# Performance work log

Measured on AMD Instinct MI355X. Metric: run time of the kernel, lower is better.

The kernel has to match this reference:

```python
import jax, jax.numpy as jnp
import numpy as np

N = 100000   # nodes
E = 3200000  # edges (avg degree 32)
D0, D1, D2, OUT = 128, 64, 64, 10


def setup_inputs() -> dict:
    key = jax.random.key(0)
    ks = jax.random.split(key, 6)
    x = jax.random.normal(ks[0], (N, D0), jnp.float32)
    edge_index = jax.random.randint(ks[1], (2, E), 0, N, jnp.int32)
    Wa1 = jax.random.normal(ks[2], (D0, D1), jnp.float32) / np.sqrt(D0).astype(np.float32)
    ba1 = jnp.zeros((D1,), jnp.float32)
    Wa2 = jax.random.normal(ks[3], (D1, D2), jnp.float32) / np.sqrt(D1).astype(np.float32)
    ba2 = jnp.zeros((D2,), jnp.float32)
    Wl = jax.random.normal(ks[4], (D2 * D2, OUT), jnp.float32) / np.sqrt(D2 * D2).astype(np.float32)
    bl = jnp.zeros((OUT,), jnp.float32)
    return {"x": x, "edge_index": edge_index, "Wa1": Wa1, "ba1": ba1,
            "Wa2": Wa2, "ba2": ba2, "Wl": Wl, "bl": bl}


def _gcn(x, W, b, src, dst, norm):
    # GCNConv: D^{-1/2} (A+I) D^{-1/2} X W + b  (self-loops already in src/dst)
    h = x @ W                                  # [N, Dout]
    m = h[src] * norm[:, None]                 # gather + scale  [E+N, Dout]
    return jax.ops.segment_sum(m, dst, num_segments=N) + b


def reference(x, edge_index, Wa1, ba1, Wa2, ba2, Wl, bl):
    loops = jnp.arange(N, dtype=edge_index.dtype)
    src = jnp.concatenate([edge_index[0], loops])
    dst = jnp.concatenate([edge_index[1], loops])
    deg = jax.ops.segment_sum(jnp.ones_like(src, jnp.float32), dst, num_segments=N)
    dinv = jax.lax.rsqrt(deg)                  # deg >= 1 thanks to self-loops
    norm = dinv[src] * dinv[dst]

    a1 = _gcn(x, Wa1, ba1, src, dst, norm)
    a2 = _gcn(a1, Wa2, ba2, src, dst, norm)
    # Original reuses gcn_a1/gcn_a2 for the x-path, so x_2 == a_2 exactly.
    x2 = a2
    h = a2.T @ x2                              # [D2, D2] attention-style readout
    o = h.reshape(1, -1) @ Wl + bl             # [1, OUT]
    return jax.nn.softmax(o, axis=-1)
```

## Files before the change

### kernel.cpp

```cpp
#include <hip/hip_runtime.h>


#define CHUNK 4096
#define BSH   8

__global__ __launch_bounds__(256) void hist_pass(const int* __restrict__ dst,
                                                 int* __restrict__ ghist,
                                                 int E, int nblk, int nbuck) {
    __shared__ int lcnt[512];
    const int blk = blockIdx.x;
    for (int i = threadIdx.x; i < nbuck; i += 256) lcnt[i] = 0;
    __syncthreads();
    const int base = blk * CHUNK;
    const int end  = min(base + CHUNK, E);
    for (int e = base + threadIdx.x; e < end; e += 256) {
        int d = __builtin_nontemporal_load(&dst[e]);
        atomicAdd(&lcnt[d >> BSH], 1);
    }
    __syncthreads();
    for (int b = threadIdx.x; b < nbuck; b += 256)
        ghist[(size_t)b * nblk + blk] = lcnt[b];
}

__global__ __launch_bounds__(256) void scan_blocks(int* __restrict__ ghist,
                                                   int* __restrict__ btot, int nblk) {
    __shared__ int sh[256];
    int* g = ghist + (size_t)blockIdx.x * nblk;
    const int tid = threadIdx.x;
    int carry = 0;
    for (int base = 0; base < nblk; base += 256) {
        int i = base + tid;
        int v = (i < nblk) ? g[i] : 0;
        sh[tid] = v;
        __syncthreads();
        for (int off = 1; off < 256; off <<= 1) {
            int t = (tid >= off) ? sh[tid - off] : 0;
            __syncthreads();
            sh[tid] += t;
            __syncthreads();
        }
        if (i < nblk) g[i] = carry + sh[tid] - v;
        int tot = sh[255];
        __syncthreads();
        carry += tot;
    }
    if (tid == 0) btot[blockIdx.x] = carry;
}

__global__ void scan_bstart(const int* __restrict__ btot, int* __restrict__ bstart, int nb) {
    __shared__ int sh[512];
    const int tid = threadIdx.x;
    int v = (tid < nb) ? btot[tid] : 0;
    sh[tid] = v;
    __syncthreads();
    for (int off = 1; off < 512; off <<= 1) {
        int t = (tid >= off) ? sh[tid - off] : 0;
        __syncthreads();
        sh[tid] += t;
        __syncthreads();
    }
    if (tid < nb) bstart[tid] = sh[tid] - v;
}

__global__ __launch_bounds__(256) void place_pass(const int* __restrict__ src,
                                                  const int* __restrict__ dst,
                                                  const int* __restrict__ ghist,
                                                  const int* __restrict__ bstart,
                                                  uint2* __restrict__ bedges,
                                                  int E, int nblk, int nbuck) {
    __shared__ int off[512];
    const int blk = blockIdx.x;
    for (int b = threadIdx.x; b < nbuck; b += 256)
        off[b] = bstart[b] + ghist[(size_t)b * nblk + blk];
    __syncthreads();
    const int base = blk * CHUNK;
    const int end  = min(base + CHUNK, E);
    for (int e = base + threadIdx.x; e < end; e += 256) {
        int d = __builtin_nontemporal_load(&dst[e]);
        int s = __builtin_nontemporal_load(&src[e]);
        int pos = atomicAdd(&off[d >> BSH], 1);
        bedges[pos] = make_uint2((unsigned)s, (unsigned)(d & 255));
    }
}

__global__ __launch_bounds__(256) void bucket_csr(const uint2* __restrict__ bedges,
                                                  const int* __restrict__ btot,
                                                  const int* __restrict__ bstart,
                                                  float* __restrict__ dinv,
                                                  int* __restrict__ rowptr,
                                                  int* __restrict__ rowend,
                                                  int* __restrict__ ssorted, int N) {
    __shared__ int lcnt[256];
    __shared__ int sc[256];
    __shared__ int lcur[256];
    const int b   = blockIdx.x;
    const int tid = threadIdx.x;
    const int cnt  = btot[b];
    const int base = bstart[b];
    lcnt[tid] = 0;
    __syncthreads();
    for (int i = tid; i < cnt; i += 256)
        atomicAdd(&lcnt[(int)bedges[base + i].y], 1);
    __syncthreads();
    int c = lcnt[tid];
    sc[tid] = c;
    __syncthreads();
    for (int off = 1; off < 256; off <<= 1) {
        int t = (tid >= off) ? sc[tid - off] : 0;
        __syncthreads();
        sc[tid] += t;
        __syncthreads();
    }
    const int excl = sc[tid] - c;
    const int n = (b << BSH) + tid;
    if (n < N) {
        dinv[n]   = rsqrtf((float)c + 1.0f);
        rowptr[n] = base + excl;
        rowend[n] = base + excl + c;
    }
    lcur[tid] = excl;
    __syncthreads();
    for (int i = tid; i < cnt; i += 256) {
        uint2 e = bedges[base + i];
        int pos = atomicAdd(&lcur[(int)e.y], 1);
        ssorted[base + pos] = (int)e.x;
    }
}

template <int K>
__global__ __launch_bounds__(256) void gemm_tiled(const float* __restrict__ A,
                                                  const float* __restrict__ W,
                                                  const float* __restrict__ dinv,
                                                  float* __restrict__ H, int N) {
    constexpr int KC = 32;
    __shared__ float xs[64][KC + 4];
    __shared__ float ws[KC][64];
    const int tid  = threadIdx.x;
    const int tx   = tid & 15;
    const int ty   = tid >> 4;
    const int base = blockIdx.x * 64;

    float acc[4][4] = {{0.f}};

    for (int kc = 0; kc < K; kc += KC) {
        for (int idx = tid; idx < 512; idx += 256) {
            int node = idx >> 3, k4 = idx & 7;
            int n = base + node;
            float4 v = make_float4(0.f, 0.f, 0.f, 0.f);
            if (n < N) v = *(const float4*)&A[(long long)n * K + kc + k4 * 4];
            *(float4*)&xs[node][k4 * 4] = v;
        }
        for (int idx = tid; idx < 512; idx += 256) {
            int k = idx >> 4, c4 = idx & 15;
            *(float4*)&ws[k][c4 * 4] = *(const float4*)&W[(long long)(kc + k) * 64 + c4 * 4];
        }
        __syncthreads();

#pragma unroll
        for (int k = 0; k < KC; k += 4) {
            float4 xv[4], wv[4];
#pragma unroll
            for (int i = 0; i < 4; ++i) xv[i] = *(const float4*)&xs[ty * 4 + i][k];
#pragma unroll
            for (int j = 0; j < 4; ++j) wv[j] = *(const float4*)&ws[k + j][tx * 4];
#pragma unroll
            for (int i = 0; i < 4; ++i) {
                float xi[4] = {xv[i].x, xv[i].y, xv[i].z, xv[i].w};
#pragma unroll
                for (int j = 0; j < 4; ++j) {
                    acc[i][0] += xi[j] * wv[j].x;
                    acc[i][1] += xi[j] * wv[j].y;
                    acc[i][2] += xi[j] * wv[j].z;
                    acc[i][3] += xi[j] * wv[j].w;
                }
            }
        }
        __syncthreads();
    }

#pragma unroll
    for (int i = 0; i < 4; ++i) {
        int n = base + ty * 4 + i;
        if (n < N) {
            float d = dinv[n];
            float4 r = make_float4(d * acc[i][0], d * acc[i][1], d * acc[i][2], d * acc[i][3]);
            *(float4*)&H[(long long)n * 64 + tx * 4] = r;
        }
    }
}

__global__ void agg_csr(const int* __restrict__ rowptr, const int* __restrict__ endptr,
                        const int* __restrict__ ssorted, const float* __restrict__ dinv,
                        const float* __restrict__ H, const float* __restrict__ bias,
                        float* __restrict__ out, int N) {
    const int wid  = (int)(((long long)blockIdx.x * blockDim.x + threadIdx.x) >> 6);
    if (wid >= N) return;
    const int lane = threadIdx.x & 63;
    const int g    = lane >> 4;
    const int fl   = lane & 15;
    const float4* __restrict__ Hv = (const float4*)H;

    const int   n   = wid;
    const int   beg = rowptr[n];
    const int   end = endptr[n];

    float4 acc = make_float4(0.f, 0.f, 0.f, 0.f);
    for (int e = beg + g; e < end; e += 4) {
        int    s  = ssorted[e];
        float4 hv = Hv[(long long)s * 16 + fl];
        acc.x += hv.x; acc.y += hv.y; acc.z += hv.z; acc.w += hv.w;
    }
    acc.x += __shfl_xor(acc.x, 16); acc.y += __shfl_xor(acc.y, 16);
    acc.z += __shfl_xor(acc.z, 16); acc.w += __shfl_xor(acc.w, 16);
    acc.x += __shfl_xor(acc.x, 32); acc.y += __shfl_xor(acc.y, 32);
    acc.z += __shfl_xor(acc.z, 32); acc.w += __shfl_xor(acc.w, 32);

    if (g == 0) {
        float4 selfv = Hv[(long long)n * 16 + fl];
        float4 bv    = ((const float4*)bias)[fl];
        float  dn    = dinv[n];
        float4 res;
        res.x = bv.x + dn * (selfv.x + acc.x);
        res.y = bv.y + dn * (selfv.y + acc.y);
        res.z = bv.z + dn * (selfv.z + acc.z);
        res.w = bv.w + dn * (selfv.w + acc.w);
        ((float4*)out)[(long long)n * 16 + fl] = res;
    }
}

__global__ void outer_reduce(const float* __restrict__ A2, float* __restrict__ h64, int N) {
    __shared__ float rows[8][64];
    const int tid = threadIdx.x;
    const int col = tid & 63;
    const int rg  = tid >> 6;
    float acc[16];
#pragma unroll
    for (int i = 0; i < 16; ++i) acc[i] = 0.f;

    int npb   = (N + gridDim.x - 1) / gridDim.x;
    int start = blockIdx.x * npb;
    int end   = min(start + npb, N);
    for (int nb = start; nb < end; nb += 8) {
        int cnt = min(8, end - nb);
        __syncthreads();
        for (int idx = tid; idx < cnt * 64; idx += 256)
            rows[idx >> 6][idx & 63] = A2[(long long)(nb + (idx >> 6)) * 64 + (idx & 63)];
        __syncthreads();
        for (int r = 0; r < cnt; ++r) {
            float vc = rows[r][col];
#pragma unroll
            for (int i = 0; i < 16; ++i)
                acc[i] += rows[r][rg * 16 + i] * vc;
        }
    }
#pragma unroll
    for (int i = 0; i < 16; ++i)
        atomicAdd(&h64[(rg * 16 + i) * 64 + col], acc[i]);
}

__global__ void final_kernel(const float* __restrict__ h64, const float* __restrict__ Wl,
                             const float* __restrict__ bl, float* __restrict__ out) {
    __shared__ float red[256];
    __shared__ float o[10];
    const int tid = threadIdx.x;
    float acc[10];
#pragma unroll
    for (int k = 0; k < 10; ++k) acc[k] = 0.f;
    for (int i = tid; i < 4096; i += 256) {
        float v = h64[i];
#pragma unroll
        for (int k = 0; k < 10; ++k) acc[k] += v * Wl[i * 10 + k];
    }
    for (int k = 0; k < 10; ++k) {
        red[tid] = acc[k];
        __syncthreads();
        for (int s = 128; s > 0; s >>= 1) {
            if (tid < s) red[tid] += red[tid + s];
            __syncthreads();
        }
        if (tid == 0) o[k] = red[0] + bl[k];
        __syncthreads();
    }
    if (tid == 0) {
        float m = o[0];
        for (int k = 1; k < 10; ++k) m = fmaxf(m, o[k]);
        float s = 0.f, e[10];
        for (int k = 0; k < 10; ++k) { e[k] = expf(o[k] - m); s += e[k]; }
        for (int k = 0; k < 10; ++k) out[k] = e[k] / s;
    }
}

extern "C" void kernel_launch(void* const* d_in, const int* in_sizes, int n_in,
                              void* d_out, int out_size, void* d_ws, size_t ws_size,
                              hipStream_t stream) {
    const float* x   = (const float*)d_in[0];
    const int*   ei  = (const int*)d_in[1];
    const float* Wa1 = (const float*)d_in[2];
    const float* ba1 = (const float*)d_in[3];
    const float* Wa2 = (const float*)d_in[4];
    const float* ba2 = (const float*)d_in[5];
    const float* Wl  = (const float*)d_in[6];
    const float* bl  = (const float*)d_in[7];
    float* out = (float*)d_out;

    const int N = in_sizes[0] / 128;
    const int E = in_sizes[1] / 2;
    const int* src = ei;
    const int* dst = ei + E;

    const int nblk  = (E + CHUNK - 1) / CHUNK;
    const int nbuck = (N + 255) >> BSH;

    char* wsb = (char*)d_ws;
    float* bufH   = (float*)wsb;
    float* bufA   = bufH + (size_t)N * 64;
    uint2* bedges = (uint2*)wsb;
    int*   ghist  = (int*)(wsb + (size_t)E * 8);
    int*   btot   = ghist + (size_t)nbuck * nblk;
    int*   bstart = btot + 512;
    char*  tail   = wsb + (size_t)N * 128 * 4;
    float* dinv   = (float*)tail;               tail += (size_t)N * 4;
    float* h64    = (float*)tail;               tail += 4096 * 4;
    int*   rowptr = (int*)tail;                 tail += (size_t)N * 4;
    int*   rowend = (int*)tail;                 tail += (size_t)N * 4;
    int*   ssorted= (int*)tail;                 tail += (size_t)E * 4;

    hist_pass<<<nblk, 256, 0, stream>>>(dst, ghist, E, nblk, nbuck);
    scan_blocks<<<nbuck, 256, 0, stream>>>(ghist, btot, nblk);
    scan_bstart<<<1, 512, 0, stream>>>(btot, bstart, nbuck);
    place_pass<<<nblk, 256, 0, stream>>>(src, dst, ghist, bstart, bedges, E, nblk, nbuck);
    bucket_csr<<<nbuck, 256, 0, stream>>>(bedges, btot, bstart, dinv, rowptr, rowend, ssorted, N);

    gemm_tiled<128><<<(N + 63) / 64, 256, 0, stream>>>(x, Wa1, dinv, bufH, N);
    agg_csr<<<(N + 3) / 4, 256, 0, stream>>>(rowptr, rowend, ssorted, dinv, bufH, ba1, bufA, N);

    gemm_tiled<64><<<(N + 63) / 64, 256, 0, stream>>>(bufA, Wa2, dinv, bufH, N);
    agg_csr<<<(N + 3) / 4, 256, 0, stream>>>(rowptr, rowend, ssorted, dinv, bufH, ba2, bufA, N);

    hipMemsetAsync(h64, 0, 4096 * sizeof(float), stream);
    outer_reduce<<<512, 256, 0, stream>>>(bufA, h64, N);
    final_kernel<<<1, 256, 0, stream>>>(h64, Wl, bl, out);
}
```

Baseline: 547.9 us.

## Shrink CSR buckets, widen aggregation gather, replace atomic outer reduce with partials

Halves the bucket width to 128 nodes so there are more buckets and more bucket_csr blocks, widening the bucket arrays and the scan to 1024 entries. The aggregation now has 8 edge groups per wavefront, each lane loading two float4s, and ssorted is read with nontemporal loads. The outer-product reduction writes per-block partials that a second kernel sums, replacing the memset and global atomics, and the final matvec uses one wavefront per output. Together these aim for more memory-level parallelism in the gather and less atomic contention, at the cost of an extra launch and a larger partial buffer.

```diff
diff --git a/kernel.cpp b/kernel.cpp
--- a/kernel.cpp
+++ b/kernel.cpp
@@ -2,12 +2,13 @@
 
 
 #define CHUNK 4096
-#define BSH   8
+#define BSH   7
+#define BMASK 127
 
 __global__ __launch_bounds__(256) void hist_pass(const int* __restrict__ dst,
                                                  int* __restrict__ ghist,
                                                  int E, int nblk, int nbuck) {
-    __shared__ int lcnt[512];
+    __shared__ int lcnt[1024];
     const int blk = blockIdx.x;
     for (int i = threadIdx.x; i < nbuck; i += 256) lcnt[i] = 0;
     __syncthreads();
@@ -48,12 +49,12 @@
 }
 
 __global__ void scan_bstart(const int* __restrict__ btot, int* __restrict__ bstart, int nb) {
-    __shared__ int sh[512];
+    __shared__ int sh[1024];
     const int tid = threadIdx.x;
     int v = (tid < nb) ? btot[tid] : 0;
     sh[tid] = v;
     __syncthreads();
-    for (int off = 1; off < 512; off <<= 1) {
+    for (int off = 1; off < 1024; off <<= 1) {
         int t = (tid >= off) ? sh[tid - off] : 0;
         __syncthreads();
         sh[tid] += t;
@@ -68,7 +69,7 @@
                                                   const int* __restrict__ bstart,
                                                   uint2* __restrict__ bedges,
                                                   int E, int nblk, int nbuck) {
-    __shared__ int off[512];
+    __shared__ int off[1024];
     const int blk = blockIdx.x;
     for (int b = threadIdx.x; b < nbuck; b += 256)
         off[b] = bstart[b] + ghist[(size_t)b * nblk + blk];
@@ -79,7 +80,7 @@
         int d = __builtin_nontemporal_load(&dst[e]);
         int s = __builtin_nontemporal_load(&src[e]);
         int pos = atomicAdd(&off[d >> BSH], 1);
-        bedges[pos] = make_uint2((unsigned)s, (unsigned)(d & 255));
+        bedges[pos] = make_uint2((unsigned)s, (unsigned)(d & BMASK));
     }
 }
 
@@ -90,35 +91,35 @@
                                                   int* __restrict__ rowptr,
                                                   int* __restrict__ rowend,
                                                   int* __restrict__ ssorted, int N) {
-    __shared__ int lcnt[256];
-    __shared__ int sc[256];
-    __shared__ int lcur[256];
+    __shared__ int lcnt[128];
+    __shared__ int sc[128];
+    __shared__ int lcur[128];
     const int b   = blockIdx.x;
     const int tid = threadIdx.x;
     const int cnt  = btot[b];
     const int base = bstart[b];
-    lcnt[tid] = 0;
+    if (tid < 128) lcnt[tid] = 0;
     __syncthreads();
     for (int i = tid; i < cnt; i += 256)
-        atomicAdd(&lcnt[(int)bedges[base + i].y], 1);
-    __syncthreads();
-    int c = lcnt[tid];
-    sc[tid] = c;
-    __syncthreads();
-    for (int off = 1; off < 256; off <<= 1) {
-        int t = (tid >= off) ? sc[tid - off] : 0;
-        __syncthreads();
-        sc[tid] += t;
-        __syncthreads();
-    }
-    const int excl = sc[tid] - c;
+        atomicAdd(&lcnt[(int)__builtin_nontemporal_load((const unsigned*)&bedges[base + i].y)], 1);
+    __syncthreads();
+    int c = (tid < 128) ? lcnt[tid] : 0;
+    if (tid < 128) sc[tid] = c;
+    __syncthreads();
+    for (int off = 1; off < 128; off <<= 1) {
+        int t = (tid >= off && tid < 128) ? sc[tid - off] : 0;
+        __syncthreads();
+        if (tid < 128) sc[tid] += t;
+        __syncthreads();
+    }
+    const int excl = (tid < 128) ? (sc[tid] - c) : 0;
     const int n = (b << BSH) + tid;
-    if (n < N) {
+    if (tid < 128 && n < N) {
         dinv[n]   = rsqrtf((float)c + 1.0f);
         rowptr[n] = base + excl;
         rowend[n] = base + excl + c;
     }
-    lcur[tid] = excl;
+    if (tid < 128) lcur[tid] = excl;
     __syncthreads();
     for (int i = tid; i < cnt; i += 256) {
         uint2 e = bedges[base + i];
@@ -196,39 +197,49 @@
     const int wid  = (int)(((long long)blockIdx.x * blockDim.x + threadIdx.x) >> 6);
     if (wid >= N) return;
     const int lane = threadIdx.x & 63;
-    const int g    = lane >> 4;
-    const int fl   = lane & 15;
+    const int g    = lane >> 3;
+    const int fl   = lane & 7;
     const float4* __restrict__ Hv = (const float4*)H;
 
-    const int   n   = wid;
-    const int   beg = rowptr[n];
-    const int   end = endptr[n];
-
-    float4 acc = make_float4(0.f, 0.f, 0.f, 0.f);
-    for (int e = beg + g; e < end; e += 4) {
-        int    s  = ssorted[e];
-        float4 hv = Hv[(long long)s * 16 + fl];
-        acc.x += hv.x; acc.y += hv.y; acc.z += hv.z; acc.w += hv.w;
-    }
-    acc.x += __shfl_xor(acc.x, 16); acc.y += __shfl_xor(acc.y, 16);
-    acc.z += __shfl_xor(acc.z, 16); acc.w += __shfl_xor(acc.w, 16);
-    acc.x += __shfl_xor(acc.x, 32); acc.y += __shfl_xor(acc.y, 32);
-    acc.z += __shfl_xor(acc.z, 32); acc.w += __shfl_xor(acc.w, 32);
+    const int n   = wid;
+    const int beg = rowptr[n];
+    const int end = endptr[n];
+
+    float4 a0 = make_float4(0.f, 0.f, 0.f, 0.f);
+    float4 a1 = make_float4(0.f, 0.f, 0.f, 0.f);
+    for (int e = beg + g; e < end; e += 8) {
+        int    s  = __builtin_nontemporal_load(&ssorted[e]);
+        float4 h0 = Hv[(long long)s * 16 + fl];
+        float4 h1 = Hv[(long long)s * 16 + fl + 8];
+        a0.x += h0.x; a0.y += h0.y; a0.z += h0.z; a0.w += h0.w;
+        a1.x += h1.x; a1.y += h1.y; a1.z += h1.z; a1.w += h1.w;
+    }
+#pragma unroll
+    for (int m = 8; m <= 32; m <<= 1) {
+        a0.x += __shfl_xor(a0.x, m); a0.y += __shfl_xor(a0.y, m);
+        a0.z += __shfl_xor(a0.z, m); a0.w += __shfl_xor(a0.w, m);
+        a1.x += __shfl_xor(a1.x, m); a1.y += __shfl_xor(a1.y, m);
+        a1.z += __shfl_xor(a1.z, m); a1.w += __shfl_xor(a1.w, m);
+    }
 
     if (g == 0) {
-        float4 selfv = Hv[(long long)n * 16 + fl];
-        float4 bv    = ((const float4*)bias)[fl];
-        float  dn    = dinv[n];
-        float4 res;
-        res.x = bv.x + dn * (selfv.x + acc.x);
-        res.y = bv.y + dn * (selfv.y + acc.y);
-        res.z = bv.z + dn * (selfv.z + acc.z);
-        res.w = bv.w + dn * (selfv.w + acc.w);
-        ((float4*)out)[(long long)n * 16 + fl] = res;
-    }
-}
-
-__global__ void outer_reduce(const float* __restrict__ A2, float* __restrict__ h64, int N) {
+        float  dn = dinv[n];
+        float4 s0 = Hv[(long long)n * 16 + fl];
+        float4 s1 = Hv[(long long)n * 16 + fl + 8];
+        float4 b0 = ((const float4*)bias)[fl];
+        float4 b1 = ((const float4*)bias)[fl + 8];
+        float4 r0, r1;
+        r0.x = b0.x + dn * (s0.x + a0.x); r0.y = b0.y + dn * (s0.y + a0.y);
+        r0.z = b0.z + dn * (s0.z + a0.z); r0.w = b0.w + dn * (s0.w + a0.w);
+        r1.x = b1.x + dn * (s1.x + a1.x); r1.y = b1.y + dn * (s1.y + a1.y);
+        r1.z = b1.z + dn * (s1.z + a1.z); r1.w = b1.w + dn * (s1.w + a1.w);
+        ((float4*)out)[(long long)n * 16 + fl]     = r0;
+        ((float4*)out)[(long long)n * 16 + fl + 8] = r1;
+    }
+}
+
+__global__ __launch_bounds__(256) void outer_partial(const float* __restrict__ A2,
+                                                     float* __restrict__ partial, int N) {
     __shared__ float rows[8][64];
     const int tid = threadIdx.x;
     const int col = tid & 63;
@@ -253,39 +264,35 @@
                 acc[i] += rows[r][rg * 16 + i] * vc;
         }
     }
+    float* p = partial + (size_t)blockIdx.x * 4096;
 #pragma unroll
     for (int i = 0; i < 16; ++i)
-        atomicAdd(&h64[(rg * 16 + i) * 64 + col], acc[i]);
+        p[(rg * 16 + i) * 64 + col] = acc[i];
+}
+
+__global__ void outer_final(const float* __restrict__ partial, float* __restrict__ h64, int nblk) {
+    int idx = blockIdx.x * blockDim.x + threadIdx.x;
+    float s = 0.f;
+    for (int b = 0; b < nblk; ++b) s += partial[(size_t)b * 4096 + idx];
+    h64[idx] = s;
 }
 
 __global__ void final_kernel(const float* __restrict__ h64, const float* __restrict__ Wl,
                              const float* __restrict__ bl, float* __restrict__ out) {
-    __shared__ float red[256];
     __shared__ float o[10];
-    const int tid = threadIdx.x;
-    float acc[10];
-#pragma unroll
-    for (int k = 0; k < 10; ++k) acc[k] = 0.f;
-    for (int i = tid; i < 4096; i += 256) {
-        float v = h64[i];
-#pragma unroll
-        for (int k = 0; k < 10; ++k) acc[k] += v * Wl[i * 10 + k];
-    }
-    for (int k = 0; k < 10; ++k) {
-        red[tid] = acc[k];
-        __syncthreads();
-        for (int s = 128; s > 0; s >>= 1) {
-            if (tid < s) red[tid] += red[tid + s];
-            __syncthreads();
-        }
-        if (tid == 0) o[k] = red[0] + bl[k];
-        __syncthreads();
-    }
-    if (tid == 0) {
-        float m = o[0];
-        for (int k = 1; k < 10; ++k) m = fmaxf(m, o[k]);
+    const int w    = threadIdx.x >> 6;
+    const int lane = threadIdx.x & 63;
+    float acc = 0.f;
+    for (int i = lane; i < 4096; i += 64) acc += h64[i] * Wl[i * 10 + w];
+#pragma unroll
+    for (int m = 1; m < 64; m <<= 1) acc += __shfl_xor(acc, m);
+    if (lane == 0) o[w] = acc + bl[w];
+    __syncthreads();
+    if (threadIdx.x == 0) {
+        float mx = o[0];
+        for (int k = 1; k < 10; ++k) mx = fmaxf(mx, o[k]);
         float s = 0.f, e[10];
-        for (int k = 0; k < 10; ++k) { e[k] = expf(o[k] - m); s += e[k]; }
+        for (int k = 0; k < 10; ++k) { e[k] = expf(o[k] - mx); s += e[k]; }
         for (int k = 0; k < 10; ++k) out[k] = e[k] / s;
     }
 }
@@ -309,15 +316,16 @@
     const int* dst = ei + E;
 
     const int nblk  = (E + CHUNK - 1) / CHUNK;
-    const int nbuck = (N + 255) >> BSH;
+    const int nbuck = (N + BMASK) >> BSH;
 
     char* wsb = (char*)d_ws;
     float* bufH   = (float*)wsb;
     float* bufA   = bufH + (size_t)N * 64;
+    float* partial= bufH;
     uint2* bedges = (uint2*)wsb;
     int*   ghist  = (int*)(wsb + (size_t)E * 8);
     int*   btot   = ghist + (size_t)nbuck * nblk;
-    int*   bstart = btot + 512;
+    int*   bstart = btot + 1024;
     char*  tail   = wsb + (size_t)N * 128 * 4;
     float* dinv   = (float*)tail;               tail += (size_t)N * 4;
     float* h64    = (float*)tail;               tail += 4096 * 4;
@@ -327,7 +335,7 @@
 
     hist_pass<<<nblk, 256, 0, stream>>>(dst, ghist, E, nblk, nbuck);
     scan_blocks<<<nbuck, 256, 0, stream>>>(ghist, btot, nblk);
-    scan_bstart<<<1, 512, 0, stream>>>(btot, bstart, nbuck);
+    scan_bstart<<<1, 1024, 0, stream>>>(btot, bstart, nbuck);
     place_pass<<<nblk, 256, 0, stream>>>(src, dst, ghist, bstart, bedges, E, nblk, nbuck);
     bucket_csr<<<nbuck, 256, 0, stream>>>(bedges, btot, bstart, dinv, rowptr, rowend, ssorted, N);
 
@@ -337,7 +345,7 @@
     gemm_tiled<64><<<(N + 63) / 64, 256, 0, stream>>>(bufA, Wa2, dinv, bufH, N);
     agg_csr<<<(N + 3) / 4, 256, 0, stream>>>(rowptr, rowend, ssorted, dinv, bufH, ba2, bufA, N);
 
-    hipMemsetAsync(h64, 0, 4096 * sizeof(float), stream);
-    outer_reduce<<<512, 256, 0, stream>>>(bufA, h64, N);
-    final_kernel<<<1, 256, 0, stream>>>(h64, Wl, bl, out);
-}
+    outer_partial<<<256, 256, 0, stream>>>(bufA, partial, N);
+    outer_final<<<16, 256, 0, stream>>>(partial, h64, 256);
+    final_kernel<<<1, 640, 0, stream>>>(h64, Wl, bl, out);
+}
```

After: 660.6 us. 20.6% more time.
